# Optimization experiments

Hardware: AMD Instinct MI355X
Metric: run time of the kernel (lower is better)

## Reference

```python
import jax, jax.numpy as jnp
import numpy as np

T, B, E, H = 1024, 2, 1024, 16
D = E // H


def setup_inputs() -> dict:
    key = jax.random.key(0)
    ks = jax.random.split(key, 5)
    s = 1.0 / np.sqrt(E)  # xavier_uniform bound ~ sqrt(6/(fan_in+fan_out)); scale suffices for a numeric baseline
    return {
        "query": jax.random.normal(ks[0], (T, B, E), jnp.float32),
        "key_": jax.random.normal(ks[1], (T, B, E), jnp.float32),
        "value": jax.random.normal(ks[2], (T, B, E), jnp.float32),
        "in_proj_weight": jax.random.uniform(ks[3], (3 * E, E), jnp.float32, -s, s),
        "in_proj_bias": jnp.zeros((3 * E,), jnp.float32),
        "out_proj_weight": jax.random.uniform(ks[4], (E, E), jnp.float32, -s, s),
        "out_proj_bias": jnp.zeros((E,), jnp.float32),
    }


def reference(query, key_, value, in_proj_weight, in_proj_bias, out_proj_weight, out_proj_bias):
    # Faithful to CumulativeLinearMultiheadAttentionKV.forward with
    # batch_first=False, is_causal=True, no padding mask, no kv cache.
    Tl, Bl, El = query.shape
    wq, wk, wv = jnp.split(in_proj_weight, 3, axis=0)
    bq, bk, bv = jnp.split(in_proj_bias, 3)
    q = query @ wq.T + bq          # (T, B, E)
    k = key_ @ wk.T + bk
    v = value @ wv.T + bv

    def to_bhtd(x):
        return x.reshape(Tl, Bl, H, D).transpose(1, 2, 0, 3)  # (B, H, T, D)

    q, k, v = to_bhtd(q), to_bhtd(k), to_bhtd(v)

    scale = 1.0 / np.sqrt(D)  # SDPA-style default scale (scale=None)
    # cumulative linear attention: prefix sums of k_s \otimes v_s
    kv = jnp.einsum('bhsk,bhsv->bhskv', k, v)        # (B, H, T, D, D)
    kv_store = jnp.cumsum(kv, axis=2)                # causal KV state per step
    out = jnp.einsum('bhtk,bhtkv->bhtv', q, kv_store) * scale  # (B, H, T, D)

    out = out.transpose(2, 0, 1, 3).reshape(Tl, Bl, El)  # back to (T, B, E)
    out = out @ out_proj_weight.T + out_proj_bias
    return out
```

## Files before the change

kernel.cpp:

```cpp
#include <hip/hip_runtime.h>


#define E_DIM 1024

typedef short bf16x8 __attribute__((ext_vector_type(8)));
typedef float f32x4  __attribute__((ext_vector_type(4)));

__device__ inline unsigned short f2bf(float f) {
    unsigned u = __builtin_bit_cast(unsigned, f);
    u = (u + 0x7FFFu + ((u >> 16) & 1u)) >> 16;
    return (unsigned short)u;
}

__device__ inline void gload_lds16(const void* g, void* l) {
    __builtin_amdgcn_global_load_lds(
        (const __attribute__((address_space(1))) unsigned int*)g,
        (__attribute__((address_space(3))) unsigned int*)l, 16, 0, 0);
}

__global__ __launch_bounds__(256) void k_cast(
    const float* __restrict__ q_in, const float* __restrict__ k_in,
    const float* __restrict__ v_in, const float* __restrict__ w_in,
    const float* __restrict__ w_out, unsigned short* __restrict__ dst)
{
    #pragma unroll
    for (int l = 0; l < 4; ++l) {
        int id8 = blockIdx.x * 256 + threadIdx.x + l * 327680;
        const float* src;
        if (id8 < 262144)        src = q_in  + (size_t)id8 * 8;
        else if (id8 < 524288)   src = k_in  + (size_t)(id8 - 262144) * 8;
        else if (id8 < 786432)   src = v_in  + (size_t)(id8 - 524288) * 8;
        else if (id8 < 1179648)  src = w_in  + (size_t)(id8 - 786432) * 8;
        else                     src = w_out + (size_t)(id8 - 1179648) * 8;
        float4 f0 = *reinterpret_cast<const float4*>(src);
        float4 f1 = *reinterpret_cast<const float4*>(src + 4);
        ushort4 o0, o1;
        o0.x = f2bf(f0.x); o0.y = f2bf(f0.y); o0.z = f2bf(f0.z); o0.w = f2bf(f0.w);
        o1.x = f2bf(f1.x); o1.y = f2bf(f1.y); o1.z = f2bf(f1.z); o1.w = f2bf(f1.w);
        *reinterpret_cast<ushort4*>(dst + (size_t)id8 * 8)     = o0;
        *reinterpret_cast<ushort4*>(dst + (size_t)id8 * 8 + 4) = o1;
    }
}

__global__ __launch_bounds__(256) void k_gin(
    const unsigned short* __restrict__ xbf, const unsigned short* __restrict__ Wibf,
    const float* __restrict__ b_in,
    unsigned short* __restrict__ qslab, unsigned short* __restrict__ kslab,
    unsigned short* __restrict__ vtb)
{
    const int i = blockIdx.x;
    const int tile = (i & 7) * 96 + (i >> 3);
    const int x = tile & 7, y = (tile >> 3) & 31, z = tile >> 8;

    const unsigned short* X = xbf + (size_t)z * 2097152;
    const unsigned short* W = Wibf + (size_t)z * 1048576;
    const float* bz = b_in + z * E_DIM;

    const int nBase = x * 128;
    const int mBase = y * 64;
    const int b = mBase >> 10, tBase = mBase & 1023;

    __shared__ short As[64 * 64];
    __shared__ short Bs[128 * 64];

    const int tid = threadIdx.x;
    const int lane = tid & 63, wave = tid >> 6;
    const int wr = wave >> 1, wc = wave & 1;
    const int l15 = lane & 15, l4 = lane >> 4;

    f32x4 acc[2][4] = {};

    for (int k0 = 0; k0 < E_DIM; k0 += 64) {
        #pragma unroll
        for (int l = 0; l < 4; ++l) {
            int off = l * 4096 + tid * 16;
            int row = off >> 7, kb = off & 127;
            gload_lds16((const char*)W + ((size_t)(nBase + row) * E_DIM + k0) * 2 + kb,
                        (char*)Bs + off);
        }
        #pragma unroll
        for (int l = 0; l < 2; ++l) {
            int off = l * 4096 + tid * 16;
            int row = off >> 7, kb = off & 127;
            gload_lds16((const char*)X +
                            ((size_t)((tBase + row) * 2 + b) * E_DIM + k0) * 2 + kb,
                        (char*)As + off);
        }
        __syncthreads();

        #pragma unroll
        for (int kk = 0; kk < 64; kk += 32) {
            bf16x8 af[2], bfr[4];
            #pragma unroll
            for (int ii = 0; ii < 2; ++ii)
                af[ii] = *reinterpret_cast<const bf16x8*>(
                            &As[(wr * 32 + ii * 16 + l15) * 64 + kk + l4 * 8]);
            #pragma unroll
            for (int j = 0; j < 4; ++j)
                bfr[j] = *reinterpret_cast<const bf16x8*>(
                            &Bs[(wc * 64 + j * 16 + l15) * 64 + kk + l4 * 8]);
            #pragma unroll
            for (int ii = 0; ii < 2; ++ii)
                #pragma unroll
                for (int j = 0; j < 4; ++j)
                    acc[ii][j] = __builtin_amdgcn_mfma_f32_16x16x32_bf16(
                        af[ii], bfr[j], acc[ii][j], 0, 0, 0);
        }
        __syncthreads();
    }

    #pragma unroll
    for (int ii = 0; ii < 2; ++ii) {
        int t0 = tBase + wr * 32 + ii * 16 + l4 * 4;
        #pragma unroll
        for (int j = 0; j < 4; ++j) {
            int col = nBase + wc * 64 + j * 16 + l15;
            float bv = bz[col];
            unsigned short v4[4];
            #pragma unroll
            for (int q = 0; q < 4; ++q) v4[q] = f2bf(acc[ii][j][q] + bv);
            if (z == 0) {
                #pragma unroll
                for (int q = 0; q < 4; ++q)
                    qslab[(size_t)b * 1048576 + (size_t)(t0 + q) * E_DIM + col] = v4[q];
            } else if (z == 1) {
                #pragma unroll
                for (int q = 0; q < 4; ++q)
                    kslab[(size_t)b * 1048576 + (size_t)(t0 + q) * E_DIM + col] = v4[q];
            } else {
                ushort4 w = {v4[0], v4[1], v4[2], v4[3]};
                *reinterpret_cast<ushort4*>(
                    &vtb[((size_t)b * 1024 + col) * 1024 + t0]) = w;
            }
        }
    }
}

__global__ __launch_bounds__(256) void k_attn(
    const unsigned short* __restrict__ qslab, const unsigned short* __restrict__ kslab,
    const unsigned short* __restrict__ vtb, unsigned short* __restrict__ attnbf)
{
    const int i = blockIdx.x;
    const int xcd = i & 7, u = i >> 3;
    const int bh = xcd * 4 + (u >> 4);
    const int qtr = u & 15;
    const int qt = ((u >> 5) & 1) ? (15 - qtr) : qtr;
    const int b = bh >> 4, h = bh & 15;
    const int colb = h * 64, t0q = qt * 64;

    __shared__ short Qs[64 * 64];
    __shared__ short Ks[64 * 64];
    __shared__ short Vts[64 * 64];
    __shared__ short Ss[64 * 72];

    const int tid = threadIdx.x;
    const int lane = tid & 63, wave = tid >> 6;
    const int wr = wave >> 1, wc = wave & 1;
    const int l15 = lane & 15, l4 = lane >> 4;

    #pragma unroll
    for (int l = 0; l < 2; ++l) {
        int off = l * 4096 + tid * 16;
        int row = off >> 7, kb = off & 127;
        gload_lds16((const char*)qslab +
                        ((size_t)b * 1048576 + (size_t)(t0q + row) * E_DIM + colb) * 2 + kb,
                    (char*)Qs + off);
    }

    f32x4 oacc[2][2] = {};

    for (int c = 0; c <= qt; ++c) {
        const int t0k = c * 64;
        #pragma unroll
        for (int l = 0; l < 2; ++l) {
            int off = l * 4096 + tid * 16;
            int row = off >> 7, kb = off & 127;
            gload_lds16((const char*)kslab +
                            ((size_t)b * 1048576 + (size_t)(t0k + row) * E_DIM + colb) * 2 + kb,
                        (char*)Ks + off);
            gload_lds16((const char*)vtb +
                            (((size_t)b * 1024 + colb + row) * 1024 + t0k) * 2 + kb,
                        (char*)Vts + off);
        }
        __syncthreads();

        f32x4 sacc[2][2] = {};
        #pragma unroll
        for (int kk = 0; kk < 64; kk += 32) {
            bf16x8 af[2], bfr[2];
            #pragma unroll
            for (int ii = 0; ii < 2; ++ii)
                af[ii] = *reinterpret_cast<const bf16x8*>(
                            &Qs[(wr * 32 + ii * 16 + l15) * 64 + kk + l4 * 8]);
            #pragma unroll
            for (int j = 0; j < 2; ++j)
                bfr[j] = *reinterpret_cast<const bf16x8*>(
                            &Ks[(wc * 32 + j * 16 + l15) * 64 + kk + l4 * 8]);
            #pragma unroll
            for (int ii = 0; ii < 2; ++ii)
                #pragma unroll
                for (int j = 0; j < 2; ++j)
                    sacc[ii][j] = __builtin_amdgcn_mfma_f32_16x16x32_bf16(
                        af[ii], bfr[j], sacc[ii][j], 0, 0, 0);
        }
        const bool diag = (c == qt);
        #pragma unroll
        for (int ii = 0; ii < 2; ++ii) {
            #pragma unroll
            for (int j = 0; j < 2; ++j) {
                int kr = wc * 32 + j * 16 + l15;
                #pragma unroll
                for (int q = 0; q < 4; ++q) {
                    int qr = wr * 32 + ii * 16 + l4 * 4 + q;
                    short sv = (short)f2bf(sacc[ii][j][q]);
                    Ss[qr * 72 + kr] = (!diag || kr <= qr) ? sv : (short)0;
                }
            }
        }
        __syncthreads();

        #pragma unroll
        for (int kk = 0; kk < 64; kk += 32) {
            bf16x8 af[2], bfr[2];
            #pragma unroll
            for (int ii = 0; ii < 2; ++ii)
                af[ii] = *reinterpret_cast<const bf16x8*>(
                            &Ss[(wr * 32 + ii * 16 + l15) * 72 + kk + l4 * 8]);
            #pragma unroll
            for (int j = 0; j < 2; ++j)
                bfr[j] = *reinterpret_cast<const bf16x8*>(
                            &Vts[(wc * 32 + j * 16 + l15) * 64 + kk + l4 * 8]);
            #pragma unroll
            for (int ii = 0; ii < 2; ++ii)
                #pragma unroll
                for (int j = 0; j < 2; ++j)
                    oacc[ii][j] = __builtin_amdgcn_mfma_f32_16x16x32_bf16(
                        af[ii], bfr[j], oacc[ii][j], 0, 0, 0);
        }
        __syncthreads();
    }

    #pragma unroll
    for (int ii = 0; ii < 2; ++ii) {
        #pragma unroll
        for (int j = 0; j < 2; ++j) {
            int dv = wc * 32 + j * 16 + l15;
            #pragma unroll
            for (int q = 0; q < 4; ++q) {
                int qr = wr * 32 + ii * 16 + l4 * 4 + q;
                attnbf[(size_t)b * 1048576 + (size_t)(t0q + qr) * E_DIM + colb + dv] =
                    f2bf(oacc[ii][j][q] * 0.125f);
            }
        }
    }
}

__global__ __launch_bounds__(256) void k_gout(
    const unsigned short* __restrict__ attnbf, const unsigned short* __restrict__ Wobf,
    const float* __restrict__ bias, float* __restrict__ out)
{
    const int i = blockIdx.x;
    const int tile = (i & 7) * 32 + (i >> 3);
    const int x = tile & 7, y = tile >> 3;
    const int nBase = x * 128;
    const int mBase = y * 64;

    __shared__ short As[64 * 64];
    __shared__ short Bs[128 * 64];

    const int tid = threadIdx.x;
    const int lane = tid & 63, wave = tid >> 6;
    const int wr = wave >> 1, wc = wave & 1;
    const int l15 = lane & 15, l4 = lane >> 4;

    f32x4 acc[2][4] = {};

    for (int k0 = 0; k0 < E_DIM; k0 += 64) {
        #pragma unroll
        for (int l = 0; l < 4; ++l) {
            int off = l * 4096 + tid * 16;
            int row = off >> 7, kb = off & 127;
            gload_lds16((const char*)Wobf + ((size_t)(nBase + row) * E_DIM + k0) * 2 + kb,
                        (char*)Bs + off);
        }
        #pragma unroll
        for (int l = 0; l < 2; ++l) {
            int off = l * 4096 + tid * 16;
            int row = off >> 7, kb = off & 127;
            int r = mBase + row, t = r >> 1, bb = r & 1;
            gload_lds16((const char*)attnbf +
                            ((size_t)bb * 1048576 + (size_t)t * E_DIM + k0) * 2 + kb,
                        (char*)As + off);
        }
        __syncthreads();

        #pragma unroll
        for (int kk = 0; kk < 64; kk += 32) {
            bf16x8 af[2], bfr[4];
            #pragma unroll
            for (int ii = 0; ii < 2; ++ii)
                af[ii] = *reinterpret_cast<const bf16x8*>(
                            &As[(wr * 32 + ii * 16 + l15) * 64 + kk + l4 * 8]);
            #pragma unroll
            for (int j = 0; j < 4; ++j)
                bfr[j] = *reinterpret_cast<const bf16x8*>(
                            &Bs[(wc * 64 + j * 16 + l15) * 64 + kk + l4 * 8]);
            #pragma unroll
            for (int ii = 0; ii < 2; ++ii)
                #pragma unroll
                for (int j = 0; j < 4; ++j)
                    acc[ii][j] = __builtin_amdgcn_mfma_f32_16x16x32_bf16(
                        af[ii], bfr[j], acc[ii][j], 0, 0, 0);
        }
        __syncthreads();
    }

    #pragma unroll
    for (int ii = 0; ii < 2; ++ii) {
        int r0 = mBase + wr * 32 + ii * 16 + l4 * 4;
        #pragma unroll
        for (int j = 0; j < 4; ++j) {
            int col = nBase + wc * 64 + j * 16 + l15;
            float bv = bias[col];
            #pragma unroll
            for (int q = 0; q < 4; ++q)
                out[(size_t)(r0 + q) * E_DIM + col] = acc[ii][j][q] + bv;
        }
    }
}

extern "C" void kernel_launch(void* const* d_in, const int* in_sizes, int n_in,
                              void* d_out, int out_size, void* d_ws, size_t ws_size,
                              hipStream_t stream)
{
    const float* q_in  = (const float*)d_in[0];
    const float* k_in  = (const float*)d_in[1];
    const float* v_in  = (const float*)d_in[2];
    const float* w_in  = (const float*)d_in[3];
    const float* b_in  = (const float*)d_in[4];
    const float* w_out = (const float*)d_in[5];
    const float* b_out = (const float*)d_in[6];

    char* w = (char*)d_ws;
    unsigned short* xbf    = (unsigned short*)w;
    unsigned short* Wibf   = (unsigned short*)(w + 12582912);
    unsigned short* Wobf   = (unsigned short*)(w + 18874368);
    unsigned short* qslab  = (unsigned short*)(w + 20971520);
    unsigned short* kslab  = (unsigned short*)(w + 25165824);
    unsigned short* vtb    = (unsigned short*)(w + 29360128);
    unsigned short* attnbf = (unsigned short*)(w + 33554432);
    float* outp = (float*)d_out;

    k_cast<<<1280, 256, 0, stream>>>(q_in, k_in, v_in, w_in, w_out, xbf);
    k_gin<<<768, 256, 0, stream>>>(xbf, Wibf, b_in, qslab, kslab, vtb);
    k_attn<<<512, 256, 0, stream>>>(qslab, kslab, vtb, attnbf);
    k_gout<<<256, 256, 0, stream>>>(attnbf, Wobf, b_out, outp);
}
```

Measured before the change: 156.5 us.

## Double-buffer LDS tiles in GEMM and attention kernels; shrink out-proj tiles

Adds two-stage LDS buffering to the input projection, attention and output projection kernels. The next K/V or A/B tile is issued through global_load_lds while MFMAs run on the current buffer, so each loop iteration needs one barrier instead of two. The output projection tile also shrinks from 64x128 to 64x64, doubling the grid to 512 blocks so more CUs are busy. In exchange, LDS use per block roughly doubles, which can lower occupancy, and the smaller tiles reuse each loaded tile less.

Result: no change. 154.0 us (-1.6%).

```diff
diff --git a/kernel.cpp b/kernel.cpp
--- a/kernel.cpp
+++ b/kernel.cpp
@@ -60,23 +60,21 @@
     const int mBase = y * 64;
     const int b = mBase >> 10, tBase = mBase & 1023;
 
-    __shared__ short As[64 * 64];
-    __shared__ short Bs[128 * 64];
+    __shared__ short As[2][64 * 64];
+    __shared__ short Bs[2][128 * 64];
 
     const int tid = threadIdx.x;
     const int lane = tid & 63, wave = tid >> 6;
     const int wr = wave >> 1, wc = wave & 1;
     const int l15 = lane & 15, l4 = lane >> 4;
 
-    f32x4 acc[2][4] = {};
-
-    for (int k0 = 0; k0 < E_DIM; k0 += 64) {
+    auto stageAB = [&](int bufI, int k0) {
         #pragma unroll
         for (int l = 0; l < 4; ++l) {
             int off = l * 4096 + tid * 16;
             int row = off >> 7, kb = off & 127;
             gload_lds16((const char*)W + ((size_t)(nBase + row) * E_DIM + k0) * 2 + kb,
-                        (char*)Bs + off);
+                        (char*)&Bs[bufI][0] + off);
         }
         #pragma unroll
         for (int l = 0; l < 2; ++l) {
@@ -84,21 +82,28 @@
             int row = off >> 7, kb = off & 127;
             gload_lds16((const char*)X +
                             ((size_t)((tBase + row) * 2 + b) * E_DIM + k0) * 2 + kb,
-                        (char*)As + off);
-        }
-        __syncthreads();
-
+                        (char*)&As[bufI][0] + off);
+        }
+    };
+
+    f32x4 acc[2][4] = {};
+
+    stageAB(0, 0);
+    __syncthreads();
+    int cur = 0;
+    for (int it = 0; it < 16; ++it) {
+        if (it < 15) stageAB(cur ^ 1, (it + 1) * 64);
         #pragma unroll
         for (int kk = 0; kk < 64; kk += 32) {
             bf16x8 af[2], bfr[4];
             #pragma unroll
             for (int ii = 0; ii < 2; ++ii)
                 af[ii] = *reinterpret_cast<const bf16x8*>(
-                            &As[(wr * 32 + ii * 16 + l15) * 64 + kk + l4 * 8]);
+                            &As[cur][(wr * 32 + ii * 16 + l15) * 64 + kk + l4 * 8]);
             #pragma unroll
             for (int j = 0; j < 4; ++j)
                 bfr[j] = *reinterpret_cast<const bf16x8*>(
-                            &Bs[(wc * 64 + j * 16 + l15) * 64 + kk + l4 * 8]);
+                            &Bs[cur][(wc * 64 + j * 16 + l15) * 64 + kk + l4 * 8]);
             #pragma unroll
             for (int ii = 0; ii < 2; ++ii)
                 #pragma unroll
@@ -107,6 +112,7 @@
                         af[ii], bfr[j], acc[ii][j], 0, 0, 0);
         }
         __syncthreads();
+        cur ^= 1;
     }
 
     #pragma unroll
@@ -149,14 +155,29 @@
     const int colb = h * 64, t0q = qt * 64;
 
     __shared__ short Qs[64 * 64];
-    __shared__ short Ks[64 * 64];
-    __shared__ short Vts[64 * 64];
+    __shared__ short Ks[2][64 * 64];
+    __shared__ short Vts[2][64 * 64];
     __shared__ short Ss[64 * 72];
 
     const int tid = threadIdx.x;
     const int lane = tid & 63, wave = tid >> 6;
     const int wr = wave >> 1, wc = wave & 1;
     const int l15 = lane & 15, l4 = lane >> 4;
+
+    auto stageKV = [&](int bufI, int c) {
+        int t0k = c * 64;
+        #pragma unroll
+        for (int l = 0; l < 2; ++l) {
+            int off = l * 4096 + tid * 16;
+            int row = off >> 7, kb = off & 127;
+            gload_lds16((const char*)kslab +
+                            ((size_t)b * 1048576 + (size_t)(t0k + row) * E_DIM + colb) * 2 + kb,
+                        (char*)&Ks[bufI][0] + off);
+            gload_lds16((const char*)vtb +
+                            (((size_t)(b * 1024 + colb + row)) * 1024 + t0k) * 2 + kb,
+                        (char*)&Vts[bufI][0] + off);
+        }
+    };
 
     #pragma unroll
     for (int l = 0; l < 2; ++l) {
@@ -166,23 +187,14 @@
                         ((size_t)b * 1048576 + (size_t)(t0q + row) * E_DIM + colb) * 2 + kb,
                     (char*)Qs + off);
     }
+    stageKV(0, 0);
+    __syncthreads();
 
     f32x4 oacc[2][2] = {};
+    int cur = 0;
 
     for (int c = 0; c <= qt; ++c) {
-        const int t0k = c * 64;
-        #pragma unroll
-        for (int l = 0; l < 2; ++l) {
-            int off = l * 4096 + tid * 16;
-            int row = off >> 7, kb = off & 127;
-            gload_lds16((const char*)kslab +
-                            ((size_t)b * 1048576 + (size_t)(t0k + row) * E_DIM + colb) * 2 + kb,
-                        (char*)Ks + off);
-            gload_lds16((const char*)vtb +
-                            (((size_t)b * 1024 + colb + row) * 1024 + t0k) * 2 + kb,
-                        (char*)Vts + off);
-        }
-        __syncthreads();
+        if (c < qt) stageKV(cur ^ 1, c + 1);
 
         f32x4 sacc[2][2] = {};
         #pragma unroll
@@ -195,7 +207,7 @@
             #pragma unroll
             for (int j = 0; j < 2; ++j)
                 bfr[j] = *reinterpret_cast<const bf16x8*>(
-                            &Ks[(wc * 32 + j * 16 + l15) * 64 + kk + l4 * 8]);
+                            &Ks[cur][(wc * 32 + j * 16 + l15) * 64 + kk + l4 * 8]);
             #pragma unroll
             for (int ii = 0; ii < 2; ++ii)
                 #pragma unroll
@@ -229,7 +241,7 @@
             #pragma unroll
             for (int j = 0; j < 2; ++j)
                 bfr[j] = *reinterpret_cast<const bf16x8*>(
-                            &Vts[(wc * 32 + j * 16 + l15) * 64 + kk + l4 * 8]);
+                            &Vts[cur][(wc * 32 + j * 16 + l15) * 64 + kk + l4 * 8]);
             #pragma unroll
             for (int ii = 0; ii < 2; ++ii)
                 #pragma unroll
@@ -238,6 +250,7 @@
                         af[ii], bfr[j], oacc[ii][j], 0, 0, 0);
         }
         __syncthreads();
+        cur ^= 1;
     }
 
     #pragma unroll
@@ -260,67 +273,68 @@
     const float* __restrict__ bias, float* __restrict__ out)
 {
     const int i = blockIdx.x;
-    const int tile = (i & 7) * 32 + (i >> 3);
-    const int x = tile & 7, y = tile >> 3;
-    const int nBase = x * 128;
+    const int tile = (i & 7) * 64 + (i >> 3);
+    const int x = tile & 15, y = tile >> 4;
+    const int nBase = x * 64;
     const int mBase = y * 64;
 
-    __shared__ short As[64 * 64];
-    __shared__ short Bs[128 * 64];
+    __shared__ short As[2][64 * 64];
+    __shared__ short Bs[2][64 * 64];
 
     const int tid = threadIdx.x;
     const int lane = tid & 63, wave = tid >> 6;
     const int wr = wave >> 1, wc = wave & 1;
     const int l15 = lane & 15, l4 = lane >> 4;
 
-    f32x4 acc[2][4] = {};
-
-    for (int k0 = 0; k0 < E_DIM; k0 += 64) {
-        #pragma unroll
-        for (int l = 0; l < 4; ++l) {
+    auto stage = [&](int bufI, int k0) {
+        #pragma unroll
+        for (int l = 0; l < 2; ++l) {
             int off = l * 4096 + tid * 16;
             int row = off >> 7, kb = off & 127;
             gload_lds16((const char*)Wobf + ((size_t)(nBase + row) * E_DIM + k0) * 2 + kb,
-                        (char*)Bs + off);
-        }
-        #pragma unroll
-        for (int l = 0; l < 2; ++l) {
-            int off = l * 4096 + tid * 16;
-            int row = off >> 7, kb = off & 127;
+                        (char*)&Bs[bufI][0] + off);
             int r = mBase + row, t = r >> 1, bb = r & 1;
             gload_lds16((const char*)attnbf +
                             ((size_t)bb * 1048576 + (size_t)t * E_DIM + k0) * 2 + kb,
-                        (char*)As + off);
-        }
-        __syncthreads();
-
+                        (char*)&As[bufI][0] + off);
+        }
+    };
+
+    f32x4 acc[2][2] = {};
+
+    stage(0, 0);
+    __syncthreads();
+    int cur = 0;
+    for (int it = 0; it < 16; ++it) {
+        if (it < 15) stage(cur ^ 1, (it + 1) * 64);
         #pragma unroll
         for (int kk = 0; kk < 64; kk += 32) {
-            bf16x8 af[2], bfr[4];
+            bf16x8 af[2], bfr[2];
             #pragma unroll
             for (int ii = 0; ii < 2; ++ii)
                 af[ii] = *reinterpret_cast<const bf16x8*>(
-                            &As[(wr * 32 + ii * 16 + l15) * 64 + kk + l4 * 8]);
-            #pragma unroll
-            for (int j = 0; j < 4; ++j)
+                            &As[cur][(wr * 32 + ii * 16 + l15) * 64 + kk + l4 * 8]);
+            #pragma unroll
+            for (int j = 0; j < 2; ++j)
                 bfr[j] = *reinterpret_cast<const bf16x8*>(
-                            &Bs[(wc * 64 + j * 16 + l15) * 64 + kk + l4 * 8]);
-            #pragma unroll
-            for (int ii = 0; ii < 2; ++ii)
-                #pragma unroll
-                for (int j = 0; j < 4; ++j)
+                            &Bs[cur][(wc * 32 + j * 16 + l15) * 64 + kk + l4 * 8]);
+            #pragma unroll
+            for (int ii = 0; ii < 2; ++ii)
+                #pragma unroll
+                for (int j = 0; j < 2; ++j)
                     acc[ii][j] = __builtin_amdgcn_mfma_f32_16x16x32_bf16(
                         af[ii], bfr[j], acc[ii][j], 0, 0, 0);
         }
         __syncthreads();
+        cur ^= 1;
     }
 
     #pragma unroll
     for (int ii = 0; ii < 2; ++ii) {
         int r0 = mBase + wr * 32 + ii * 16 + l4 * 4;
         #pragma unroll
-        for (int j = 0; j < 4; ++j) {
-            int col = nBase + wc * 64 + j * 16 + l15;
+        for (int j = 0; j < 2; ++j) {
+            int col = nBase + wc * 32 + j * 16 + l15;
             float bv = bias[col];
             #pragma unroll
             for (int q = 0; q < 4; ++q)
@@ -354,5 +368,5 @@
     k_cast<<<1280, 256, 0, stream>>>(q_in, k_in, v_in, w_in, w_out, xbf);
     k_gin<<<768, 256, 0, stream>>>(xbf, Wibf, b_in, qslab, kslab, vtb);
     k_attn<<<512, 256, 0, stream>>>(qslab, kslab, vtb, attnbf);
-    k_gout<<<256, 256, 0, stream>>>(attnbf, Wobf, b_out, outp);
-}
+    k_gout<<<512, 256, 0, stream>>>(attnbf, Wobf, b_out, outp);
+}
```
